# Optimization experiments

Hardware: AMD Instinct MI355X
Metric: run time of the kernel (lower is better)

Reference implementation:

```python
import jax, jax.numpy as jnp
import numpy as np

N = 100000      # nodes
E = 800000      # edges (avg degree 8)
D_IN = 128
D_OUT = 128
HOPS = 3        # K in SGConv


def setup_inputs() -> dict:
    key = jax.random.key(0)
    k1, k2, k3 = jax.random.split(key, 3)
    x = jax.random.normal(k1, (N, D_IN), dtype=jnp.float32)
    edge_index = jax.random.randint(k2, (2, E), 0, N, dtype=jnp.int64)
    # SGConv's final torch.nn.Linear(in_channels, out_channels)
    W = jax.random.normal(k3, (D_OUT, D_IN), dtype=jnp.float32) / np.sqrt(D_IN).astype(np.float32)
    b = jnp.zeros((D_OUT,), dtype=jnp.float32)
    return {"x": x, "edge_index": edge_index, "W": W, "b": b}


def reference(x, edge_index, W, b):
    n = x.shape[0]
    loop = jnp.arange(n, dtype=edge_index.dtype)
    # gcn_norm with add_self_loops=True (SGConv default)
    src = jnp.concatenate([edge_index[0], loop])  # message sources
    dst = jnp.concatenate([edge_index[1], loop])  # aggregation targets
    ones = jnp.ones(src.shape[0], dtype=x.dtype)
    deg = jax.ops.segment_sum(ones, dst, num_segments=n)
    dinv = jnp.where(deg > 0, jax.lax.rsqrt(deg), 0.0)
    norm = dinv[src] * dinv[dst]  # symmetric D^-1/2 A_hat D^-1/2 coefficients

    def hop(h, _):
        msg = h[src] * norm[:, None]                      # [E+N, D] gather
        return jax.ops.segment_sum(msg, dst, num_segments=n), None

    h, _ = jax.lax.scan(hop, x, None, length=HOPS)        # A_norm^K x
    return h @ W.T + b                                     # final linear
```

## Files before the change

kernel.cpp:

```cpp
#include <hip/hip_runtime.h>
#include <hip/hip_bf16.h>

#define DF 128
#define CAP 32
#define OVF_CAP 65536


typedef __attribute__((ext_vector_type(8))) short shortx8;
typedef __attribute__((ext_vector_type(4))) float floatx4;

__device__ __forceinline__ unsigned short f32_to_bf16_rne(float f) {
    unsigned int u = __float_as_uint(f);
    unsigned int r = (u >> 16) & 1u;
    u += 0x7FFFu + r;
    return (unsigned short)(u >> 16);
}
__device__ __forceinline__ float bf16_lo(unsigned int w) { return __uint_as_float(w << 16); }
__device__ __forceinline__ float bf16_hi(unsigned int w) { return __uint_as_float(w & 0xffff0000u); }
__device__ __forceinline__ unsigned int pack_bf16(float x, float y) {
    return ((unsigned int)f32_to_bf16_rne(y) << 16) | (unsigned int)f32_to_bf16_rne(x);
}

__global__ void detect_flags_kernel(const unsigned int* __restrict__ ew, int enwords,
                                    const unsigned short* __restrict__ xh, int xnh,
                                    int* __restrict__ flagI, int* __restrict__ flagD) {
    __shared__ int eodd_nz;
    __shared__ int xbig;
    if (threadIdx.x == 0) { eodd_nz = 0; xbig = 0; }
    __syncthreads();
    int f1 = 0;
    for (int i = 1 + 2 * (int)threadIdx.x; i < enwords; i += 2 * (int)blockDim.x)
        if (ew[i] != 0u) f1 = 1;
    int c = 0;
    for (int i = 2 * (int)threadIdx.x; i < xnh; i += 2 * (int)blockDim.x) {
        unsigned int e = ((unsigned int)xh[i] >> 7) & 0xFFu;
        if (e >= 0xC0u) c++;
    }
    if (f1) eodd_nz = 1;
    if (c) atomicAdd(&xbig, c);
    __syncthreads();
    if (threadIdx.x == 0) {
        *flagI = (eodd_nz == 0) ? 1 : 0;
        *flagD = (xbig > 8) ? 0 : 1;
    }
}

__global__ __launch_bounds__(256) void prep_kernel(
        const int* __restrict__ eidx, const int* __restrict__ flagI,
        const int* __restrict__ flagD, int E, int n,
        int* __restrict__ cnt, int* __restrict__ csrF,
        int2* __restrict__ ovf, int* __restrict__ ovf_cnt,
        const void* __restrict__ x, uint2* __restrict__ xb, int nw2,
        const void* __restrict__ W, const void* __restrict__ b,
        unsigned short* __restrict__ Wb, float* __restrict__ bias_f,
        int g1, int g2) {
    int bid = (int)blockIdx.x;
    if (bid < g1) {
        int t = bid * 256 + (int)threadIdx.x;
        int base = t * 8;
        if (base >= E) return;
        int isI64 = *flagI;
        const long long* p64 = (const long long*)eidx;
        int s[8], d[8];
#pragma unroll
        for (int j = 0; j < 8; ++j) {
            int e = base + j;
            if (e < E) {
                if (isI64) { s[j] = (int)p64[e]; d[j] = (int)p64[(long long)E + e]; }
                else       { s[j] = eidx[e];     d[j] = eidx[E + e]; }
            } else { s[j] = -1; d[j] = -1; }
        }
        int r[8];
#pragma unroll
        for (int j = 0; j < 8; ++j) {
            bool ok = ((unsigned)d[j] < (unsigned)n) && ((unsigned)s[j] < (unsigned)n);
            r[j] = ok ? atomicAdd(&cnt[d[j]], 1) : -1;
        }
#pragma unroll
        for (int j = 0; j < 8; ++j) {
            if (r[j] < 0) continue;
            if (r[j] < CAP) {
                __builtin_nontemporal_store(s[j], &csrF[d[j] * CAP + r[j]]);
            } else {
                int p = atomicAdd(ovf_cnt, 1);
                if (p < OVF_CAP) ovf[p] = make_int2(s[j], d[j]);
            }
        }
    } else if (bid < g1 + g2) {
        int i = (bid - g1) * 256 + (int)threadIdx.x;
        if (i >= nw2) return;
        if (*flagD) {
            xb[i] = ((const uint2*)x)[i];
        } else {
            float4 v = ((const float4*)x)[i];
            uint2 o;
            o.x = pack_bf16(v.x, v.y);
            o.y = pack_bf16(v.z, v.w);
            xb[i] = o;
        }
    } else {
        int i = (bid - g1 - g2) * 256 + (int)threadIdx.x;
        int bf = *flagD;
        if (i < 128 * 128)
            Wb[i] = bf ? ((const unsigned short*)W)[i] : f32_to_bf16_rne(((const float*)W)[i]);
        if (i < 128)
            bias_f[i] = bf ? bf16_lo((unsigned int)((const unsigned short*)b)[i]) : ((const float*)b)[i];
    }
}

__global__ __launch_bounds__(256) void hop_kernel(const uint4* __restrict__ hin,
                                                  uint4* __restrict__ hout,
                                                  const int* __restrict__ csrF,
                                                  const int* __restrict__ cnt, int n) {
    int gw = (int)((blockIdx.x * 256 + threadIdx.x) >> 6);
    int lane = (int)(threadIdx.x & 63);
    if (gw >= n) return;
    int e = lane >> 4, c = lane & 15;
    int cv = cnt[gw];
    float di = rsqrtf((float)(cv + 1));
    int beg = gw * CAP;
    int len = cv < CAP ? cv : CAP;
    int end = beg + len;
    uint4 sv = hin[(size_t)gw * 16 + c];
    float a0 = 0.f, a1 = 0.f, a2 = 0.f, a3 = 0.f, a4 = 0.f, a5 = 0.f, a6 = 0.f, a7 = 0.f;
    for (int j = beg + e; j < end; j += 8) {
        int s0 = csrF[j];
        bool has1 = (j + 4) < end;
        int s1 = has1 ? csrF[j + 4] : s0;
        uint4 v0 = hin[(size_t)s0 * 16 + c];
        uint4 v1 = hin[(size_t)s1 * 16 + c];
        float w0 = rsqrtf((float)(cnt[s0] + 1));
        float w1 = has1 ? rsqrtf((float)(cnt[s1] + 1)) : 0.f;
        a0 += w0 * bf16_lo(v0.x); a1 += w0 * bf16_hi(v0.x);
        a2 += w0 * bf16_lo(v0.y); a3 += w0 * bf16_hi(v0.y);
        a4 += w0 * bf16_lo(v0.z); a5 += w0 * bf16_hi(v0.z);
        a6 += w0 * bf16_lo(v0.w); a7 += w0 * bf16_hi(v0.w);
        a0 += w1 * bf16_lo(v1.x); a1 += w1 * bf16_hi(v1.x);
        a2 += w1 * bf16_lo(v1.y); a3 += w1 * bf16_hi(v1.y);
        a4 += w1 * bf16_lo(v1.z); a5 += w1 * bf16_hi(v1.z);
        a6 += w1 * bf16_lo(v1.w); a7 += w1 * bf16_hi(v1.w);
    }
    a0 += __shfl_xor(a0, 16); a0 += __shfl_xor(a0, 32);
    a1 += __shfl_xor(a1, 16); a1 += __shfl_xor(a1, 32);
    a2 += __shfl_xor(a2, 16); a2 += __shfl_xor(a2, 32);
    a3 += __shfl_xor(a3, 16); a3 += __shfl_xor(a3, 32);
    a4 += __shfl_xor(a4, 16); a4 += __shfl_xor(a4, 32);
    a5 += __shfl_xor(a5, 16); a5 += __shfl_xor(a5, 32);
    a6 += __shfl_xor(a6, 16); a6 += __shfl_xor(a6, 32);
    a7 += __shfl_xor(a7, 16); a7 += __shfl_xor(a7, 32);
    a0 = di * (a0 + di * bf16_lo(sv.x)); a1 = di * (a1 + di * bf16_hi(sv.x));
    a2 = di * (a2 + di * bf16_lo(sv.y)); a3 = di * (a3 + di * bf16_hi(sv.y));
    a4 = di * (a4 + di * bf16_lo(sv.z)); a5 = di * (a5 + di * bf16_hi(sv.z));
    a6 = di * (a6 + di * bf16_lo(sv.w)); a7 = di * (a7 + di * bf16_hi(sv.w));
    if (e == 0) {
        uint4 o;
        o.x = pack_bf16(a0, a1);
        o.y = pack_bf16(a2, a3);
        o.z = pack_bf16(a4, a5);
        o.w = pack_bf16(a6, a7);
        hout[(size_t)gw * 16 + c] = o;
    }
}

__global__ void fixup_kernel(const unsigned int* __restrict__ hin,
                             unsigned int* __restrict__ hout,
                             const int2* __restrict__ ovf, const int* __restrict__ ovf_cnt,
                             const int* __restrict__ cnt) {
    int m = *ovf_cnt;
    if (m > OVF_CAP) m = OVF_CAP;
    int t = (int)threadIdx.x;
    for (int i = 0; i < m; ++i) {
        int2 sd = ovf[i];
        float w  = rsqrtf((float)(cnt[sd.x] + 1));
        float dd = rsqrtf((float)(cnt[sd.y] + 1));
        unsigned int hv = hin[(size_t)sd.x * 64 + t];
        unsigned int ov = hout[(size_t)sd.y * 64 + t];
        float lo = bf16_lo(ov) + dd * w * bf16_lo(hv);
        float hi = bf16_hi(ov) + dd * w * bf16_hi(hv);
        hout[(size_t)sd.y * 64 + t] = pack_bf16(lo, hi);
    }
}

__global__ __launch_bounds__(256, 2) void linear_mfma_kernel(
        const unsigned short* __restrict__ h, const unsigned short* __restrict__ Wb,
        const float* __restrict__ bias_f, void* __restrict__ out,
        const int* __restrict__ flagD, int n) {
    int bf = *flagD;
    int wave = (int)(threadIdx.x >> 6);
    int lane = (int)(threadIdx.x & 63);
    int q = lane >> 4, m16 = lane & 15;

    shortx8 bfrag[8][4];
    float bias[8];
#pragma unroll
    for (int nt = 0; nt < 8; ++nt) {
        int wr = nt * 16 + m16;
#pragma unroll
        for (int t = 0; t < 4; ++t)
            bfrag[nt][t] = *(const shortx8*)&Wb[wr * 128 + t * 32 + q * 8];
        bias[nt] = bias_f[wr];
    }

    int nstrips = (n + 15) / 16;
    int wid = (int)blockIdx.x * 4 + wave;
    int nw = (int)gridDim.x * 4;
    for (int s = wid; s < nstrips; s += nw) {
        int row0 = s * 16;
        int arow = row0 + m16;
        if (arow >= n) arow = n - 1;
        shortx8 afrag[4];
#pragma unroll
        for (int t = 0; t < 4; ++t)
            afrag[t] = *(const shortx8*)&h[(size_t)arow * 128 + t * 32 + q * 8];

        floatx4 acc[8];
#pragma unroll
        for (int nt = 0; nt < 8; ++nt) acc[nt] = (floatx4){0.f, 0.f, 0.f, 0.f};
#pragma unroll
        for (int t = 0; t < 4; ++t)
#pragma unroll
            for (int nt = 0; nt < 8; ++nt)
                acc[nt] = __builtin_amdgcn_mfma_f32_16x16x32_bf16(afrag[t], bfrag[nt][t], acc[nt], 0, 0, 0);

#pragma unroll
        for (int nt = 0; nt < 8; ++nt)
#pragma unroll
            for (int r = 0; r < 4; ++r) {
                int row = row0 + q * 4 + r;
                if (row < n) {
                    float v = acc[nt][r] + bias[nt];
                    size_t oi = (size_t)row * 128 + nt * 16 + m16;
                    if (bf) ((unsigned short*)out)[oi] = f32_to_bf16_rne(v);
                    else    ((float*)out)[oi] = v;
                }
            }
    }
}

extern "C" void kernel_launch(void* const* d_in, const int* in_sizes, int n_in,
                              void* d_out, int out_size, void* d_ws, size_t ws_size,
                              hipStream_t stream) {
    const void* x = d_in[0];
    const int* eidx = (const int*)d_in[1];
    const void* W = d_in[2];
    const void* b = d_in[3];

    int n = in_sizes[0] / DF;
    int E = in_sizes[1] / 2;

    char* ws = (char*)d_ws;
    size_t off = 0;
    auto alloc = [&](size_t bytes) -> void* {
        void* p = ws + off;
        off = (off + bytes + 255) & ~(size_t)255;
        return p;
    };
    unsigned int* hb = (unsigned int*)alloc((size_t)n * 64 * 4);
    int*   cnt       = (int*)alloc((size_t)n * 4);
    int*   flagI     = (int*)alloc(256);
    int*   flagD     = (int*)alloc(256);
    unsigned short* Wb = (unsigned short*)alloc(128 * 128 * 2);
    float* bias_f    = (float*)alloc(128 * 4);
    int*   csrF      = (int*)alloc((size_t)n * CAP * 4);
    int2*  ovf       = (int2*)alloc((size_t)OVF_CAP * 8);
    int*   ovf_cnt   = (int*)alloc(256);
    unsigned int* xb = (unsigned int*)d_out;

    hipMemsetAsync(cnt, 0, (size_t)n * 4, stream);
    hipMemsetAsync(ovf_cnt, 0, 4, stream);

    int enw = 8192; if (2 * E < enw) enw = 2 * E;
    int xnh = 16384; if (n * DF < xnh) xnh = n * DF;
    detect_flags_kernel<<<1, 256, 0, stream>>>((const unsigned int*)eidx, enw,
                                               (const unsigned short*)x, xnh, flagI, flagD);

    int e8 = (E + 7) / 8;
    int g1 = (e8 + 255) / 256;
    int nw2 = n * 32;
    int g2 = (nw2 + 255) / 256;
    int g3 = 64;

    prep_kernel<<<g1 + g2 + g3, 256, 0, stream>>>(
        eidx, flagI, flagD, E, n, cnt, csrF, ovf, ovf_cnt,
        x, (uint2*)xb, nw2, W, b, Wb, bias_f, g1, g2);

    int hb_grid = (n + 3) / 4;
    hop_kernel<<<hb_grid, 256, 0, stream>>>((const uint4*)xb, (uint4*)hb, csrF, cnt, n);
    fixup_kernel<<<1, 64, 0, stream>>>((const unsigned int*)xb, hb, ovf, ovf_cnt, cnt);
    hop_kernel<<<hb_grid, 256, 0, stream>>>((const uint4*)hb, (uint4*)xb, csrF, cnt, n);
    fixup_kernel<<<1, 64, 0, stream>>>((const unsigned int*)hb, xb, ovf, ovf_cnt, cnt);
    hop_kernel<<<hb_grid, 256, 0, stream>>>((const uint4*)xb, (uint4*)hb, csrF, cnt, n);
    fixup_kernel<<<1, 64, 0, stream>>>((const unsigned int*)xb, hb, ovf, ovf_cnt, cnt);

    int nstrips = (n + 15) / 16;
    int lgrid = 512; if ((nstrips + 3) / 4 < lgrid) lgrid = (nstrips + 3) / 4;
    linear_mfma_kernel<<<lgrid, 256, 0, stream>>>(
        (const unsigned short*)hb, Wb, bias_f, d_out, flagD, n);
}
```

Baseline: 319.5 us.

## Fold overflow fixup into hop kernel and merge memsets into init kernel

Removes the three single-block fixup launches by having each hop wave whose node has more than CAP in-edges scan the overflow list and add the extra contributions before the reduction. The two memsets and the flag-detection kernel are merged into one init kernel that also zeroes the degree counts and the overflow counter. This cuts several launches and serial single-block work from the critical path. The cost is that high-degree nodes now do a linear scan over the whole overflow list on every hop, which is slow if overflow is common.

```diff
diff --git a/kernel.cpp b/kernel.cpp
--- a/kernel.cpp
+++ b/kernel.cpp
@@ -21,27 +21,40 @@
     return ((unsigned int)f32_to_bf16_rne(y) << 16) | (unsigned int)f32_to_bf16_rne(x);
 }
 
-__global__ void detect_flags_kernel(const unsigned int* __restrict__ ew, int enwords,
-                                    const unsigned short* __restrict__ xh, int xnh,
-                                    int* __restrict__ flagI, int* __restrict__ flagD) {
-    __shared__ int eodd_nz;
-    __shared__ int xbig;
-    if (threadIdx.x == 0) { eodd_nz = 0; xbig = 0; }
-    __syncthreads();
-    int f1 = 0;
-    for (int i = 1 + 2 * (int)threadIdx.x; i < enwords; i += 2 * (int)blockDim.x)
-        if (ew[i] != 0u) f1 = 1;
-    int c = 0;
-    for (int i = 2 * (int)threadIdx.x; i < xnh; i += 2 * (int)blockDim.x) {
-        unsigned int e = ((unsigned int)xh[i] >> 7) & 0xFFu;
-        if (e >= 0xC0u) c++;
-    }
-    if (f1) eodd_nz = 1;
-    if (c) atomicAdd(&xbig, c);
-    __syncthreads();
-    if (threadIdx.x == 0) {
-        *flagI = (eodd_nz == 0) ? 1 : 0;
-        *flagD = (xbig > 8) ? 0 : 1;
+__global__ __launch_bounds__(256) void init_kernel(const unsigned int* __restrict__ ew, int enwords,
+                                                   const unsigned short* __restrict__ xh, int xnh,
+                                                   int* __restrict__ flagI, int* __restrict__ flagD,
+                                                   int* __restrict__ cnt, int n,
+                                                   int* __restrict__ ovf_cnt) {
+    int bid = (int)blockIdx.x;
+    if (bid == 0) {
+        __shared__ int eodd_nz;
+        __shared__ int xbig;
+        if (threadIdx.x == 0) { eodd_nz = 0; xbig = 0; }
+        __syncthreads();
+        int f1 = 0;
+        for (int i = 1 + 2 * (int)threadIdx.x; i < enwords; i += 2 * (int)blockDim.x)
+            if (ew[i] != 0u) f1 = 1;
+        int c = 0;
+        for (int i = 2 * (int)threadIdx.x; i < xnh; i += 2 * (int)blockDim.x) {
+            unsigned int e = ((unsigned int)xh[i] >> 7) & 0xFFu;
+            if (e >= 0xC0u) c++;
+        }
+        if (f1) eodd_nz = 1;
+        if (c) atomicAdd(&xbig, c);
+        __syncthreads();
+        if (threadIdx.x == 0) {
+            *flagI = (eodd_nz == 0) ? 1 : 0;
+            *flagD = (xbig > 8) ? 0 : 1;
+            *ovf_cnt = 0;
+        }
+    } else {
+        int n4 = n >> 2;
+        int i = (bid - 1) * 256 + (int)threadIdx.x;
+        if (i < n4) ((int4*)cnt)[i] = make_int4(0, 0, 0, 0);
+        int tail0 = n4 << 2;
+        int t = tail0 + i;
+        if (i < 4 && t < n) cnt[t] = 0;
     }
 }
 
@@ -111,7 +124,9 @@
 __global__ __launch_bounds__(256) void hop_kernel(const uint4* __restrict__ hin,
                                                   uint4* __restrict__ hout,
                                                   const int* __restrict__ csrF,
-                                                  const int* __restrict__ cnt, int n) {
+                                                  const int* __restrict__ cnt,
+                                                  const int2* __restrict__ ovf,
+                                                  const int* __restrict__ ovf_cnt, int n) {
     int gw = (int)((blockIdx.x * 256 + threadIdx.x) >> 6);
     int lane = (int)(threadIdx.x & 63);
     if (gw >= n) return;
@@ -140,6 +155,19 @@
         a4 += w1 * bf16_lo(v1.z); a5 += w1 * bf16_hi(v1.z);
         a6 += w1 * bf16_lo(v1.w); a7 += w1 * bf16_hi(v1.w);
     }
+    if (cv > CAP && e == 0) {
+        int m = *ovf_cnt; if (m > OVF_CAP) m = OVF_CAP;
+        for (int i = 0; i < m; ++i) {
+            int2 ov = ovf[i];
+            if (ov.y != gw) continue;
+            float w = rsqrtf((float)(cnt[ov.x] + 1));
+            uint4 v = hin[(size_t)ov.x * 16 + c];
+            a0 += w * bf16_lo(v.x); a1 += w * bf16_hi(v.x);
+            a2 += w * bf16_lo(v.y); a3 += w * bf16_hi(v.y);
+            a4 += w * bf16_lo(v.z); a5 += w * bf16_hi(v.z);
+            a6 += w * bf16_lo(v.w); a7 += w * bf16_hi(v.w);
+        }
+    }
     a0 += __shfl_xor(a0, 16); a0 += __shfl_xor(a0, 32);
     a1 += __shfl_xor(a1, 16); a1 += __shfl_xor(a1, 32);
     a2 += __shfl_xor(a2, 16); a2 += __shfl_xor(a2, 32);
@@ -162,25 +190,6 @@
     }
 }
 
-__global__ void fixup_kernel(const unsigned int* __restrict__ hin,
-                             unsigned int* __restrict__ hout,
-                             const int2* __restrict__ ovf, const int* __restrict__ ovf_cnt,
-                             const int* __restrict__ cnt) {
-    int m = *ovf_cnt;
-    if (m > OVF_CAP) m = OVF_CAP;
-    int t = (int)threadIdx.x;
-    for (int i = 0; i < m; ++i) {
-        int2 sd = ovf[i];
-        float w  = rsqrtf((float)(cnt[sd.x] + 1));
-        float dd = rsqrtf((float)(cnt[sd.y] + 1));
-        unsigned int hv = hin[(size_t)sd.x * 64 + t];
-        unsigned int ov = hout[(size_t)sd.y * 64 + t];
-        float lo = bf16_lo(ov) + dd * w * bf16_lo(hv);
-        float hi = bf16_hi(ov) + dd * w * bf16_hi(hv);
-        hout[(size_t)sd.y * 64 + t] = pack_bf16(lo, hi);
-    }
-}
-
 __global__ __launch_bounds__(256, 2) void linear_mfma_kernel(
         const unsigned short* __restrict__ h, const unsigned short* __restrict__ Wb,
         const float* __restrict__ bias_f, void* __restrict__ out,
@@ -266,13 +275,13 @@
     int*   ovf_cnt   = (int*)alloc(256);
     unsigned int* xb = (unsigned int*)d_out;
 
-    hipMemsetAsync(cnt, 0, (size_t)n * 4, stream);
-    hipMemsetAsync(ovf_cnt, 0, 4, stream);
-
     int enw = 8192; if (2 * E < enw) enw = 2 * E;
     int xnh = 16384; if (n * DF < xnh) xnh = n * DF;
-    detect_flags_kernel<<<1, 256, 0, stream>>>((const unsigned int*)eidx, enw,
-                                               (const unsigned short*)x, xnh, flagI, flagD);
+
+    int nzb = ((n >> 2) + 255) / 256;
+    init_kernel<<<1 + nzb, 256, 0, stream>>>((const unsigned int*)eidx, enw,
+                                             (const unsigned short*)x, xnh,
+                                             flagI, flagD, cnt, n, ovf_cnt);
 
     int e8 = (E + 7) / 8;
     int g1 = (e8 + 255) / 256;
@@ -285,12 +294,9 @@
         x, (uint2*)xb, nw2, W, b, Wb, bias_f, g1, g2);
 
     int hb_grid = (n + 3) / 4;
-    hop_kernel<<<hb_grid, 256, 0, stream>>>((const uint4*)xb, (uint4*)hb, csrF, cnt, n);
-    fixup_kernel<<<1, 64, 0, stream>>>((const unsigned int*)xb, hb, ovf, ovf_cnt, cnt);
-    hop_kernel<<<hb_grid, 256, 0, stream>>>((const uint4*)hb, (uint4*)xb, csrF, cnt, n);
-    fixup_kernel<<<1, 64, 0, stream>>>((const unsigned int*)hb, xb, ovf, ovf_cnt, cnt);
-    hop_kernel<<<hb_grid, 256, 0, stream>>>((const uint4*)xb, (uint4*)hb, csrF, cnt, n);
-    fixup_kernel<<<1, 64, 0, stream>>>((const unsigned int*)xb, hb, ovf, ovf_cnt, cnt);
+    hop_kernel<<<hb_grid, 256, 0, stream>>>((const uint4*)xb, (uint4*)hb, csrF, cnt, ovf, ovf_cnt, n);
+    hop_kernel<<<hb_grid, 256, 0, stream>>>((const uint4*)hb, (uint4*)xb, csrF, cnt, ovf, ovf_cnt, n);
+    hop_kernel<<<hb_grid, 256, 0, stream>>>((const uint4*)xb, (uint4*)hb, csrF, cnt, ovf, ovf_cnt, n);
 
     int nstrips = (n + 15) / 16;
     int lgrid = 512; if ((nstrips + 3) / 4 < lgrid) lgrid = (nstrips + 3) / 4;
```

Result: faster. 311.8 us (-2.4%).
